# Optimization experiments

Measured on AMD Instinct MI355X. Metric: run time of the kernel, lower is better.

## Reference

```python
import jax, jax.numpy as jnp
import numpy as np

D_MODEL = 1024
N_HEAD = 16
D_K = D_MODEL // N_HEAD
MAX_LEN = 1000
LN_EPS = 1e-5


def setup_inputs() -> dict:
    key = jax.random.key(0)
    ks = jax.random.split(key, 12)
    B, S = 4, 1000
    def xavier(k, shape):
        fan_in, fan_out = shape[1], shape[0]
        lim = np.sqrt(6.0 / (fan_in + fan_out))
        return jax.random.uniform(k, shape, jnp.float32, -lim, lim)
    return {
        "q": jax.random.normal(ks[0], (B, S, D_MODEL), jnp.float32),
        "k": jax.random.normal(ks[1], (B, S, D_MODEL), jnp.float32),
        "v": jax.random.normal(ks[2], (B, S, D_MODEL), jnp.float32),
        "ln_g": jnp.ones((D_MODEL,), jnp.float32),
        "ln_b": jnp.zeros((D_MODEL,), jnp.float32),
        "wq": xavier(ks[3], (D_MODEL, D_MODEL)),
        "bq": jnp.zeros((D_MODEL,), jnp.float32),
        "wk": xavier(ks[4], (D_MODEL, D_MODEL)),
        "bk": jnp.zeros((D_MODEL,), jnp.float32),
        "wv": xavier(ks[5], (D_MODEL, D_MODEL)),
        "bv": jnp.zeros((D_MODEL,), jnp.float32),
        "wo": xavier(ks[6], (D_MODEL, D_MODEL)),
        "bo": jnp.zeros((D_MODEL,), jnp.float32),
        "rel_emb": jax.random.normal(ks[7], (2 * MAX_LEN - 1, D_K), jnp.float32) / np.sqrt(D_K),
    }


def _layer_norm(x, g, b):
    mu = jnp.mean(x, axis=-1, keepdims=True)
    var = jnp.mean(jnp.square(x - mu), axis=-1, keepdims=True)
    return (x - mu) * jax.lax.rsqrt(var + LN_EPS) * g + b


def reference(q, k, v, ln_g, ln_b, wq, bq, wk, bk, wv, bv, wo, bo, rel_emb):
    B, S, _ = q.shape
    residual = q
    qn = _layer_norm(q, ln_g, ln_b)
    kn = _layer_norm(k, ln_g, ln_b)
    vn = _layer_norm(v, ln_g, ln_b)
    # torch Linear: y = x @ W^T + b; reshape to [B, H, S, d_k]
    def proj(x, w, b):
        return (x @ w.T + b).reshape(B, S, N_HEAD, D_K).transpose(0, 2, 1, 3)
    qh = proj(qn, wq, bq)
    kh = proj(kn, wk, bk)
    vh = proj(vn, wv, bv)
    scale = 1.0 / np.sqrt(D_K)
    scores = jnp.einsum('bhid,bhjd->bhij', qh, kh) * scale
    # relative position bias: rel_pos[i, j] = emb[center + (i - j)]
    center = MAX_LEN - 1
    start = center - (S - 1)
    window = jax.lax.dynamic_slice_in_dim(rel_emb, start, 2 * S - 1, axis=0)  # [2S-1, d_k]
    pos = jnp.arange(S)
    rel_idx = pos[:, None] - pos[None, :] + (S - 1)  # [S, S] in [0, 2S-2]
    rel_pos = window[rel_idx]  # [S, S, d_k]
    scores = scores + jnp.einsum('bhik,ijk->bhij', qh, rel_pos) * scale
    attn = jax.nn.softmax(scores, axis=-1)
    out = jnp.einsum('bhij,bhjd->bhid', attn, vh)
    out = out.transpose(0, 2, 1, 3).reshape(B, S, D_MODEL)
    out = out @ wo.T + bo
    return out + residual
```

## Files before the change

### kernel.cpp

```cpp
#include <hip/hip_runtime.h>
#include <hip/hip_bf16.h>

#define D_MODEL 1024
#define N_HEAD  16
#define D_K     64
#define MAX_LEN 1000
#define B_      4
#define S_      1000
#define S_PAD   1024
#define M_PAD   (B_ * S_PAD)
#define M_REAL  (B_ * S_)
#define LN_EPS  1e-5f
#define SCALE_L2E 0.1803368801111204f
#define REL_ROWS (2*MAX_LEN-1)

typedef __attribute__((ext_vector_type(8))) short short8;
typedef __attribute__((ext_vector_type(4))) float f32x4;

__device__ __forceinline__ unsigned short f2b(float f) {
    unsigned u = __builtin_bit_cast(unsigned, f);
    u = (u + 0x7FFFu + ((u >> 16) & 1u)) >> 16;
    return (unsigned short)u;
}

__device__ __forceinline__ unsigned short f2b_trunc(float f) {
    return (unsigned short)(__builtin_bit_cast(unsigned, f) >> 16);
}

__device__ __forceinline__ float b2f(unsigned short u) {
    return __builtin_bit_cast(float, (unsigned)u << 16);
}

__device__ __forceinline__ f32x4 mfma16(short8 a, short8 b, f32x4 c) {
    return __builtin_amdgcn_mfma_f32_16x16x32_bf16(a, b, c, 0, 0, 0);
}

__device__ __forceinline__ void gload_lds16(const void* g, void* l) {
    __builtin_amdgcn_global_load_lds(
        (const __attribute__((address_space(1))) unsigned int*)g,
        (__attribute__((address_space(3))) unsigned int*)l, 16, 0, 0);
}

__global__ void cvt_all(const float* __restrict__ s0, const float* __restrict__ s1,
                        const float* __restrict__ s2, const float* __restrict__ s3,
                        const float* __restrict__ s4,
                        unsigned short* __restrict__ d0, unsigned short* __restrict__ d1,
                        unsigned short* __restrict__ d2, unsigned short* __restrict__ d3,
                        unsigned short* __restrict__ d4) {
    int y = blockIdx.y;
    const float* in; unsigned short* out; int n4;
    switch (y) {
        case 0: in = s0; out = d0; n4 = 262144; break;
        case 1: in = s1; out = d1; n4 = 262144; break;
        case 2: in = s2; out = d2; n4 = 262144; break;
        case 3: in = s3; out = d3; n4 = 262144; break;
        default: in = s4; out = d4; n4 = REL_ROWS * D_K / 4; break;
    }
    int i = blockIdx.x * blockDim.x + threadIdx.x;
    if (i >= n4) return;
    float4 v = ((const float4*)in)[i];
    ushort4 o;
    o.x = f2b(v.x); o.y = f2b(v.y); o.z = f2b(v.z); o.w = f2b(v.w);
    ((ushort4*)out)[i] = o;
}

__global__ void ln_all(const float* __restrict__ xq, const float* __restrict__ xk,
                       const float* __restrict__ xv, const float* __restrict__ g,
                       const float* __restrict__ beta,
                       unsigned short* __restrict__ yq, unsigned short* __restrict__ yk,
                       unsigned short* __restrict__ yv) {
    int which = blockIdx.y;
    const float* x = which == 0 ? xq : which == 1 ? xk : xv;
    unsigned short* y = which == 0 ? yq : which == 1 ? yk : yv;

    int r = blockIdx.x;
    int b = r >> 10, i = r & 1023;
    unsigned short* yr = y + (size_t)r * D_MODEL;
    int tid = threadIdx.x;
    if (i >= S_) {
#pragma unroll
        for (int l = 0; l < 4; ++l) yr[tid + l * 256] = 0;
        return;
    }
    const float* xr = x + ((size_t)b * S_ + i) * D_MODEL;
    float v[4];
    float s = 0.f, sq = 0.f;
#pragma unroll
    for (int l = 0; l < 4; ++l) {
        v[l] = xr[tid + l * 256];
        s += v[l];
        sq += v[l] * v[l];
    }
#pragma unroll
    for (int o = 32; o > 0; o >>= 1) {
        s += __shfl_down(s, o, 64);
        sq += __shfl_down(sq, o, 64);
    }
    __shared__ float rs[4], rq[4];
    if ((tid & 63) == 0) { rs[tid >> 6] = s; rq[tid >> 6] = sq; }
    __syncthreads();
    if (tid == 0) {
        rs[0] = rs[0] + rs[1] + rs[2] + rs[3];
        rq[0] = rq[0] + rq[1] + rq[2] + rq[3];
    }
    __syncthreads();
    float mu = rs[0] * (1.0f / D_MODEL);
    float var = rq[0] * (1.0f / D_MODEL) - mu * mu;
    float rstd = rsqrtf(var + LN_EPS);
#pragma unroll
    for (int l = 0; l < 4; ++l) {
        int c = tid + l * 256;
        yr[c] = f2b((v[l] - mu) * rstd * g[c] + beta[c]);
    }
}

template<int MODE>
__device__ __forceinline__ void gemm_body(
        const unsigned short* __restrict__ X, const unsigned short* __restrict__ W,
        const float* __restrict__ bias, const float* __restrict__ resid,
        unsigned short* __restrict__ Yb, float* __restrict__ Yf,
        unsigned short* As, unsigned short* Bs, int row0, int col0) {
    int tid = threadIdx.x;
    int lane = tid & 63, w = tid >> 6;
    int wr = w >> 1, wc = w & 1;
    int fr = lane & 15, fk = (lane >> 4) * 8;

    f32x4 acc[4][4];
#pragma unroll
    for (int fm = 0; fm < 4; ++fm)
#pragma unroll
        for (int fn = 0; fn < 4; ++fn) acc[fm][fn] = (f32x4)0.f;

    int c0 = (w * 2 + 0) * 64 + lane;
    int c1 = (w * 2 + 1) * 64 + lane;
    const unsigned short* xs0 = X + (size_t)(row0 + (c0 >> 2)) * 1024 + (c0 & 3) * 8;
    const unsigned short* xs1 = X + (size_t)(row0 + (c1 >> 2)) * 1024 + (c1 & 3) * 8;
    const unsigned short* ws0 = W + (size_t)(col0 + (c0 >> 2)) * 1024 + (c0 & 3) * 8;
    const unsigned short* ws1 = W + (size_t)(col0 + (c1 >> 2)) * 1024 + (c1 & 3) * 8;
    unsigned short* ad0 = As + (w * 2 + 0) * 512;
    unsigned short* ad1 = As + (w * 2 + 1) * 512;
    unsigned short* bd0 = Bs + (w * 2 + 0) * 512;
    unsigned short* bd1 = Bs + (w * 2 + 1) * 512;

    for (int k0 = 0; k0 < 1024; k0 += 32) {
        gload_lds16(xs0 + k0, ad0);
        gload_lds16(xs1 + k0, ad1);
        gload_lds16(ws0 + k0, bd0);
        gload_lds16(ws1 + k0, bd1);
        __syncthreads();
        short8 a[4], b[4];
#pragma unroll
        for (int fm = 0; fm < 4; ++fm)
            a[fm] = *(const short8*)(As + (wr * 64 + fm * 16 + fr) * 32 + fk);
#pragma unroll
        for (int fn = 0; fn < 4; ++fn)
            b[fn] = *(const short8*)(Bs + (wc * 64 + fn * 16 + fr) * 32 + fk);
#pragma unroll
        for (int fm = 0; fm < 4; ++fm)
#pragma unroll
            for (int fn = 0; fn < 4; ++fn)
                acc[fm][fn] = mfma16(a[fm], b[fn], acc[fm][fn]);
        __syncthreads();
    }

#pragma unroll
    for (int fm = 0; fm < 4; ++fm) {
#pragma unroll
        for (int fn = 0; fn < 4; ++fn) {
            int cg = col0 + wc * 64 + fn * 16 + fr;
            float bv = bias[cg];
#pragma unroll
            for (int r = 0; r < 4; ++r) {
                int rg = row0 + wr * 64 + fm * 16 + (lane >> 4) * 4 + r;
                float val = acc[fm][fn][r] + bv;
                int b_ = rg >> 10, i = rg & 1023;
                if (MODE == 0) {
                    int h = cg >> 6, d = cg & 63;
                    Yb[(((size_t)(b_ * N_HEAD + h)) * S_PAD + i) * D_K + d] = f2b(val);
                } else if (MODE == 1) {
                    int h = cg >> 6, d = cg & 63;
                    Yb[(((size_t)(b_ * N_HEAD + h)) * D_K + d) * S_PAD + i] = f2b(val);
                } else {
                    if (i < S_) {
                        size_t orow = (size_t)b_ * S_ + i;
                        Yf[orow * 1024 + cg] = val + resid[orow * 1024 + cg];
                    }
                }
            }
        }
    }
}

__global__ __launch_bounds__(256) void gemm_qkv(
        const unsigned short* __restrict__ qn, const unsigned short* __restrict__ kn,
        const unsigned short* __restrict__ vn,
        const unsigned short* __restrict__ wqb, const unsigned short* __restrict__ wkb,
        const unsigned short* __restrict__ wvb,
        const float* __restrict__ bq, const float* __restrict__ bk,
        const float* __restrict__ bv,
        unsigned short* __restrict__ qh, unsigned short* __restrict__ kh,
        unsigned short* __restrict__ vt) {
    __shared__ __align__(16) unsigned short As[128 * 32];
    __shared__ __align__(16) unsigned short Bs[128 * 32];
    int z = blockIdx.z;
    int row0 = blockIdx.y * 128, col0 = blockIdx.x * 128;
    if (z == 0)
        gemm_body<0>(qn, wqb, bq, nullptr, qh, nullptr, As, Bs, row0, col0);
    else if (z == 1)
        gemm_body<0>(kn, wkb, bk, nullptr, kh, nullptr, As, Bs, row0, col0);
    else
        gemm_body<1>(vn, wvb, bv, nullptr, vt, nullptr, As, Bs, row0, col0);
}

__global__ __launch_bounds__(256) void gemm_out(
        const unsigned short* __restrict__ X, const unsigned short* __restrict__ W,
        const float* __restrict__ bias, const float* __restrict__ resid,
        float* __restrict__ Yf) {
    __shared__ __align__(16) unsigned short As[128 * 32];
    __shared__ __align__(16) unsigned short Bs[128 * 32];
    gemm_body<2>(X, W, bias, resid, nullptr, Yf, As, Bs, blockIdx.y * 128, blockIdx.x * 128);
}

#define QRW 84
#define PW  72
__device__ __forceinline__ void attn_slab(
        const unsigned short* __restrict__ Kc, const unsigned short* __restrict__ Vc,
        unsigned short* __restrict__ qp, const short8 (*rl)[2],
        short8 aq0, short8 aq1, f32x4* accO, float* mrun, float* lrun,
        bool mask_needed, int j0, int fr, int fk8, int rgrp, int rsw) {
    f32x4 accS[4];
#pragma unroll
    for (int fj = 0; fj < 4; ++fj) accS[fj] = (f32x4)0.f;
    __builtin_amdgcn_s_setprio(1);
#pragma unroll
    for (int fj = 0; fj < 4; ++fj) {
        int kb = (fj * 16 + fr) * 64 + fk8;
        accS[fj] = mfma16(aq0, *(const short8*)(Kc + (kb ^ rsw)), accS[fj]);
        accS[fj] = mfma16(aq1, *(const short8*)(Kc + ((kb + 32) ^ rsw)), accS[fj]);
    }
#pragma unroll
    for (int fu = 0; fu < 5; ++fu) {
        f32x4 qr = (f32x4)0.f;
        qr = mfma16(aq0, rl[fu][0], qr);
        qr = mfma16(aq1, rl[fu][1], qr);
#pragma unroll
        for (int r = 0; r < 4; ++r)
            qp[(rgrp + r) * QRW + fu * 16 + fr] = f2b_trunc(qr[r]);
    }
    __builtin_amdgcn_s_setprio(0);

    float sc[4][4];
#pragma unroll
    for (int fj = 0; fj < 4; ++fj) {
        int j_loc = fj * 16 + fr;
#pragma unroll
        for (int r = 0; r < 4; ++r) {
            int col = rgrp + r - j_loc + 63;
            sc[fj][r] = (accS[fj][r] + b2f(qp[(rgrp + r) * QRW + col])) * SCALE_L2E;
        }
    }
    if (mask_needed) {
#pragma unroll
        for (int fj = 0; fj < 4; ++fj) {
            int j_loc = fj * 16 + fr;
            if (j0 + j_loc >= S_) {
#pragma unroll
                for (int r = 0; r < 4; ++r) sc[fj][r] = -3e38f;
            }
        }
    }

    float pm[4];
#pragma unroll
    for (int r = 0; r < 4; ++r)
        pm[r] = fmaxf(fmaxf(sc[0][r], sc[1][r]), fmaxf(sc[2][r], sc[3][r]));
#pragma unroll
    for (int mask = 1; mask <= 8; mask <<= 1)
#pragma unroll
        for (int r = 0; r < 4; ++r)
            pm[r] = fmaxf(pm[r], __shfl_xor(pm[r], mask, 64));

    float dmax = fmaxf(fmaxf(pm[0] - mrun[0], pm[1] - mrun[1]),
                       fmaxf(pm[2] - mrun[2], pm[3] - mrun[3]));
    if (!__all(dmax <= 8.0f)) {
#pragma unroll
        for (int r = 0; r < 4; ++r) {
            float mn = fmaxf(mrun[r], pm[r]);
            float scl = __builtin_amdgcn_exp2f(mrun[r] - mn);
            mrun[r] = mn;
            lrun[r] *= scl;
#pragma unroll
            for (int fd = 0; fd < 4; ++fd) accO[fd][r] *= scl;
        }
    }

    float rsum[4];
#pragma unroll
    for (int r = 0; r < 4; ++r) rsum[r] = 0.f;
#pragma unroll
    for (int fj = 0; fj < 4; ++fj) {
#pragma unroll
        for (int r = 0; r < 4; ++r) {
            float p = __builtin_amdgcn_exp2f(sc[fj][r] - mrun[r]);
            rsum[r] += p;
            qp[(rgrp + r) * PW + fj * 16 + fr] = f2b_trunc(p);
        }
    }
#pragma unroll
    for (int mask = 1; mask <= 8; mask <<= 1)
#pragma unroll
        for (int r = 0; r < 4; ++r)
            rsum[r] += __shfl_xor(rsum[r], mask, 64);
#pragma unroll
    for (int r = 0; r < 4; ++r) lrun[r] += rsum[r];

    short8 ap0 = *(const short8*)(qp + fr * PW + fk8);
    short8 ap1 = *(const short8*)(qp + fr * PW + 32 + fk8);
    __builtin_amdgcn_s_setprio(1);
#pragma unroll
    for (int fd = 0; fd < 4; ++fd) {
        int vb = (fd * 16 + fr) * 64 + fk8;
        accO[fd] = mfma16(ap0, *(const short8*)(Vc + (vb ^ rsw)), accO[fd]);
        accO[fd] = mfma16(ap1, *(const short8*)(Vc + ((vb + 32) ^ rsw)), accO[fd]);
    }
    __builtin_amdgcn_s_setprio(0);
}

__global__ __launch_bounds__(256, 2) void attn_mfma(
        const unsigned short* __restrict__ qh, const unsigned short* __restrict__ kh,
        const unsigned short* __restrict__ vt, const unsigned short* __restrict__ relb,
        unsigned short* __restrict__ aout) {
    __shared__ __align__(16) unsigned short Ks[2][64 * 64];
    __shared__ __align__(16) unsigned short Vs[2][64 * 64];
    __shared__ __align__(16) unsigned short QP[4][16 * QRW];

    int tid = threadIdx.x, lane = tid & 63, w = tid >> 6;
    int bid = blockIdx.x;
    int swz = (bid & 7) * 64 + (bid >> 3);
    int bh = swz >> 3;
    int i0a = (((swz & 7) * 8) + 2 * w) * 16;
    int fr = lane & 15, fk8 = (lane >> 4) * 8, rgrp = (lane >> 4) * 4;
    int rsw = (fr & 7) << 3;

    const unsigned short* kbase = kh + (size_t)bh * S_PAD * D_K;
    const unsigned short* vtbase = vt + (size_t)bh * D_K * S_PAD;

    const unsigned short* qpa = qh + ((size_t)bh * S_PAD + i0a + fr) * D_K + fk8;
    short8 aqa0 = *(const short8*)(qpa);
    short8 aqa1 = *(const short8*)(qpa + 32);
    const unsigned short* qpb = qpa + 16 * D_K;
    short8 aqb0 = *(const short8*)(qpb);
    short8 aqb1 = *(const short8*)(qpb + 32);

    f32x4 accOa[4], accOb[4];
    float mruna[4], lruna[4], mrunb[4], lrunb[4];
#pragma unroll
    for (int fd = 0; fd < 4; ++fd) { accOa[fd] = (f32x4)0.f; accOb[fd] = (f32x4)0.f; }
#pragma unroll
    for (int r = 0; r < 4; ++r) {
        mruna[r] = -3e38f; lruna[r] = 0.f;
        mrunb[r] = -3e38f; lrunb[r] = 0.f;
    }

    unsigned short* qp = QP[w];
    int row_in = lane >> 3, slot = lane & 7;

    auto stage = [&](int buf, int it2) {
        int j0s = it2 * 64;
#pragma unroll
        for (int cc = 0; cc < 2; ++cc) {
            int c = w * 2 + cc;
            int r = c * 8 + row_in;
            gload_lds16(kbase + (size_t)(j0s + r) * 64 + (slot ^ row_in) * 8,
                        &Ks[buf][c * 512]);
        }
#pragma unroll
        for (int cc = 0; cc < 2; ++cc) {
            int c = w * 2 + cc;
            int d = c * 8 + row_in;
            gload_lds16(vtbase + (size_t)d * S_PAD + j0s + (slot ^ row_in) * 8,
                        &Vs[buf][c * 512]);
        }
    };

    stage(0, 0);
    __syncthreads();

    for (int it = 0; it < 16; ++it) {
        int cur = it & 1, j0 = it * 64;
        bool mask_needed = (j0 + 63 >= S_);

        short8 rl[6][2];
        int ub = i0a - j0 + (S_ - D_K);
#pragma unroll
        for (int fu = 0; fu < 6; ++fu) {
            int u = ub + fu * 16 + fr;
            u = u < 0 ? 0 : (u > REL_ROWS - 1 ? REL_ROWS - 1 : u);
            const unsigned short* rp = relb + (size_t)u * D_K + fk8;
            rl[fu][0] = *(const short8*)(rp);
            rl[fu][1] = *(const short8*)(rp + 32);
        }
        __builtin_amdgcn_sched_barrier(0);

        if (it < 15) stage(cur ^ 1, it + 1);

        attn_slab(Ks[cur], Vs[cur], qp, rl, aqa0, aqa1, accOa, mruna, lruna,
                  mask_needed, j0, fr, fk8, rgrp, rsw);
        attn_slab(Ks[cur], Vs[cur], qp, rl + 1, aqb0, aqb1, accOb, mrunb, lrunb,
                  mask_needed, j0, fr, fk8, rgrp, rsw);

        __syncthreads();
    }

    int b_ = bh >> 4, h = bh & 15;
#pragma unroll
    for (int r = 0; r < 4; ++r) {
        float inva = 1.0f / lruna[r];
        float invb = 1.0f / lrunb[r];
        int ma = b_ * S_PAD + i0a + rgrp + r;
        int mb = ma + 16;
#pragma unroll
        for (int fd = 0; fd < 4; ++fd) {
            int c = h * D_K + fd * 16 + fr;
            aout[(size_t)ma * D_MODEL + c] = f2b(accOa[fd][r] * inva);
            aout[(size_t)mb * D_MODEL + c] = f2b(accOb[fd][r] * invb);
        }
    }
}

extern "C" void kernel_launch(void* const* d_in, const int* in_sizes, int n_in,
                              void* d_out, int out_size, void* d_ws, size_t ws_size,
                              hipStream_t stream) {
    const float* q    = (const float*)d_in[0];
    const float* k    = (const float*)d_in[1];
    const float* v    = (const float*)d_in[2];
    const float* ln_g = (const float*)d_in[3];
    const float* ln_b = (const float*)d_in[4];
    const float* wq   = (const float*)d_in[5];
    const float* bq   = (const float*)d_in[6];
    const float* wk   = (const float*)d_in[7];
    const float* bk   = (const float*)d_in[8];
    const float* wv   = (const float*)d_in[9];
    const float* bv   = (const float*)d_in[10];
    const float* wo   = (const float*)d_in[11];
    const float* bo   = (const float*)d_in[12];
    const float* rel  = (const float*)d_in[13];
    float* out = (float*)d_out;

    const size_t TSZ = (size_t)M_PAD * D_MODEL;
    unsigned short* ws   = (unsigned short*)d_ws;
    unsigned short* qn   = ws;
    unsigned short* kn   = qn + TSZ;
    unsigned short* vn   = kn + TSZ;
    unsigned short* qh   = vn + TSZ;
    unsigned short* kh   = qh + TSZ;
    unsigned short* vt   = kh + TSZ;
    unsigned short* aout = vt + TSZ;
    unsigned short* wqb  = aout + TSZ;
    unsigned short* wkb  = wqb + 1024 * 1024;
    unsigned short* wvb  = wkb + 1024 * 1024;
    unsigned short* wob  = wvb + 1024 * 1024;
    unsigned short* relb = wob + 1024 * 1024;

    cvt_all<<<dim3(1024, 5), 256, 0, stream>>>(wq, wk, wv, wo, rel,
                                               wqb, wkb, wvb, wob, relb);

    ln_all<<<dim3(M_PAD, 3), 256, 0, stream>>>(q, k, v, ln_g, ln_b, qn, kn, vn);

    gemm_qkv<<<dim3(8, 32, 3), 256, 0, stream>>>(qn, kn, vn, wqb, wkb, wvb,
                                                 bq, bk, bv, qh, kh, vt);

    attn_mfma<<<512, 256, 0, stream>>>(qh, kh, vt, relb, aout);

    gemm_out<<<dim3(8, 32), 256, 0, stream>>>(aout, wob, bo, q, out);
}
```

Before: 197.0 us.

## Double-buffer GEMM LDS staging and swizzle block-to-tile mapping

The projection GEMM main loop now uses two LDS buffers, issuing the next K-slice's global-to-LDS loads before computing on the current one and dropping one barrier per iteration. The block index is also remapped so that consecutive workgroups spread across row tiles, which is meant to improve cache reuse and spread load across XCDs. Together these aim to hide global-load latency behind MFMA work. In exchange the kernel uses twice the LDS, which may lower occupancy, and with a single barrier per iteration the buffer reuse depends on the async LDS loads being ordered correctly.

```diff
diff --git a/kernel.cpp b/kernel.cpp
--- a/kernel.cpp
+++ b/kernel.cpp
@@ -137,30 +137,36 @@
     const unsigned short* xs1 = X + (size_t)(row0 + (c1 >> 2)) * 1024 + (c1 & 3) * 8;
     const unsigned short* ws0 = W + (size_t)(col0 + (c0 >> 2)) * 1024 + (c0 & 3) * 8;
     const unsigned short* ws1 = W + (size_t)(col0 + (c1 >> 2)) * 1024 + (c1 & 3) * 8;
-    unsigned short* ad0 = As + (w * 2 + 0) * 512;
-    unsigned short* ad1 = As + (w * 2 + 1) * 512;
-    unsigned short* bd0 = Bs + (w * 2 + 0) * 512;
-    unsigned short* bd1 = Bs + (w * 2 + 1) * 512;
-
-    for (int k0 = 0; k0 < 1024; k0 += 32) {
-        gload_lds16(xs0 + k0, ad0);
-        gload_lds16(xs1 + k0, ad1);
-        gload_lds16(ws0 + k0, bd0);
-        gload_lds16(ws1 + k0, bd1);
+    int do0 = (w * 2 + 0) * 512;
+    int do1 = (w * 2 + 1) * 512;
+
+    auto stage = [&](int buf, int k0) {
+        gload_lds16(xs0 + k0, As + buf * 4096 + do0);
+        gload_lds16(xs1 + k0, As + buf * 4096 + do1);
+        gload_lds16(ws0 + k0, Bs + buf * 4096 + do0);
+        gload_lds16(ws1 + k0, Bs + buf * 4096 + do1);
+    };
+
+    stage(0, 0);
+
+    for (int it = 0; it < 32; ++it) {
         __syncthreads();
+        if (it < 31) stage((it & 1) ^ 1, (it + 1) * 32);
+
+        const unsigned short* Ab = As + (it & 1) * 4096;
+        const unsigned short* Bb = Bs + (it & 1) * 4096;
         short8 a[4], b[4];
 #pragma unroll
         for (int fm = 0; fm < 4; ++fm)
-            a[fm] = *(const short8*)(As + (wr * 64 + fm * 16 + fr) * 32 + fk);
+            a[fm] = *(const short8*)(Ab + (wr * 64 + fm * 16 + fr) * 32 + fk);
 #pragma unroll
         for (int fn = 0; fn < 4; ++fn)
-            b[fn] = *(const short8*)(Bs + (wc * 64 + fn * 16 + fr) * 32 + fk);
+            b[fn] = *(const short8*)(Bb + (wc * 64 + fn * 16 + fr) * 32 + fk);
 #pragma unroll
         for (int fm = 0; fm < 4; ++fm)
 #pragma unroll
             for (int fn = 0; fn < 4; ++fn)
                 acc[fm][fn] = mfma16(a[fm], b[fn], acc[fm][fn]);
-        __syncthreads();
     }
 
 #pragma unroll
@@ -200,25 +206,31 @@
         const float* __restrict__ bv,
         unsigned short* __restrict__ qh, unsigned short* __restrict__ kh,
         unsigned short* __restrict__ vt) {
-    __shared__ __align__(16) unsigned short As[128 * 32];
-    __shared__ __align__(16) unsigned short Bs[128 * 32];
-    int z = blockIdx.z;
-    int row0 = blockIdx.y * 128, col0 = blockIdx.x * 128;
-    if (z == 0)
-        gemm_body<0>(qn, wqb, bq, nullptr, qh, nullptr, As, Bs, row0, col0);
-    else if (z == 1)
-        gemm_body<0>(kn, wkb, bk, nullptr, kh, nullptr, As, Bs, row0, col0);
+    __shared__ __align__(16) unsigned short As[2][128 * 32];
+    __shared__ __align__(16) unsigned short Bs[2][128 * 32];
+    int fid = blockIdx.x + (blockIdx.y << 3) + (blockIdx.z << 8);
+    int swz = (fid & 7) * 96 + (fid >> 3);
+    int bz = swz >> 8;
+    int rem = swz & 255;
+    int row0 = (rem >> 3) * 128, col0 = (rem & 7) * 128;
+    if (bz == 0)
+        gemm_body<0>(qn, wqb, bq, nullptr, qh, nullptr, As[0], Bs[0], row0, col0);
+    else if (bz == 1)
+        gemm_body<0>(kn, wkb, bk, nullptr, kh, nullptr, As[0], Bs[0], row0, col0);
     else
-        gemm_body<1>(vn, wvb, bv, nullptr, vt, nullptr, As, Bs, row0, col0);
+        gemm_body<1>(vn, wvb, bv, nullptr, vt, nullptr, As[0], Bs[0], row0, col0);
 }
 
 __global__ __launch_bounds__(256) void gemm_out(
         const unsigned short* __restrict__ X, const unsigned short* __restrict__ W,
         const float* __restrict__ bias, const float* __restrict__ resid,
         float* __restrict__ Yf) {
-    __shared__ __align__(16) unsigned short As[128 * 32];
-    __shared__ __align__(16) unsigned short Bs[128 * 32];
-    gemm_body<2>(X, W, bias, resid, nullptr, Yf, As, Bs, blockIdx.y * 128, blockIdx.x * 128);
+    __shared__ __align__(16) unsigned short As[2][128 * 32];
+    __shared__ __align__(16) unsigned short Bs[2][128 * 32];
+    int fid = blockIdx.x + (blockIdx.y << 3);
+    int swz = (fid & 7) * 32 + (fid >> 3);
+    int row0 = (swz >> 3) * 128, col0 = (swz & 7) * 128;
+    gemm_body<2>(X, W, bias, resid, nullptr, Yf, As[0], Bs[0], row0, col0);
 }
 
 #define QRW 84
```

Result: faster. 181.5 us (-7.9%).
